# Kernel tuning notes

Hardware: AMD Instinct MI355X
Metric: run time of the kernel (lower is better)

## Reference

```python
import jax, jax.numpy as jnp
import numpy as np

B = 32768          # number of document embeddings
EMB = 768          # emb_size
M = 32             # subvector_num
K = 256            # subvector_cents = 2**subvector_bits
D = EMB // M       # last_dim per subvector = 24


def setup_inputs() -> dict:
    key = jax.random.key(0)
    k1, k2, k3 = jax.random.split(key, 3)
    x = jax.random.normal(k1, (B, EMB), dtype=jnp.float32)
    codebook = jax.random.normal(k2, (M, K, D), dtype=jnp.float32) * 0.05
    # OPQ rotation matrix (orthogonal-ish init; stored as a frozen Parameter in torch)
    rotate = jax.random.normal(k3, (EMB, EMB), dtype=jnp.float32) / np.sqrt(EMB)
    return {"x": x, "codebook": codebook, "rotate": rotate}


def reference(x, codebook, rotate):
    # OPQ: rotate embeddings first (torch: torch.matmul(cur_embeddings, self.rotate.T))
    xr = jnp.matmul(x, rotate.T)                      # [B, EMB]
    # Split into subvectors: [B, M, D]
    xs = xr.reshape(B, M, D)
    # dist_mode == 'ip': compute_scores = sum(a * b, -1) per subvector per centroid
    scores = jnp.einsum('bmd,mkd->bmk', xs, codebook)  # [B, M, K]
    return scores
```

## Files before the change

### kernel.cpp

```cpp
#include <hip/hip_runtime.h>
#include <hip/hip_bf16.h>

typedef __bf16 bf16;
typedef __bf16 bf16x4 __attribute__((ext_vector_type(4)));
typedef __bf16 bf16x8 __attribute__((ext_vector_type(8)));
typedef float f32x4 __attribute__((ext_vector_type(4)));

#define NB   32768
#define EMB  768
#define MSUB 32
#define KC   256
#define DSUB 24


__device__ __forceinline__ bf16x8 cvt8(float4 a, float4 b) {
    bf16x8 r;
    r[0] = (bf16)a.x; r[1] = (bf16)a.y; r[2] = (bf16)a.z; r[3] = (bf16)a.w;
    r[4] = (bf16)b.x; r[5] = (bf16)b.y; r[6] = (bf16)b.z; r[7] = (bf16)b.w;
    return r;
}

__device__ __forceinline__ void lds_barrier() {
    asm volatile("s_waitcnt lgkmcnt(0)" ::: "memory");
    __builtin_amdgcn_s_barrier();
    __builtin_amdgcn_sched_barrier(0);
}

__global__ __launch_bounds__(256, 4)
void pq_prep(const float* __restrict__ cb, const float* __restrict__ rot,
             bf16* __restrict__ cb_pad, bf16* __restrict__ rot_f) {
    const int b = blockIdx.x;
    const int t = threadIdx.x;
    if (b < 288) {
        const int o     = b * 2048 + t * 8;
        const int chunk = o >> 9;
        const int lane8 = o & 511;
        const int l15   = (lane8 >> 3) & 15;
        const int lg    = lane8 >> 7;
        const int jj    = (chunk / 24) * 16 + l15;
        const int ee    = (chunk % 24) * 32 + lg * 8;
        const float* rp = rot + (size_t)jj * EMB + ee;
        *(bf16x8*)(rot_f + o) = cvt8(*(const float4*)rp, *(const float4*)(rp + 4));
    } else {
        const int o  = (b - 288) * 2048 + t * 8;
        const int m  = o >> 13;
        const int k  = (o >> 5) & 255;
        const int d0 = o & 31;
        bf16x8 v;
        if (d0 < DSUB) {
            const float* cp = cb + (size_t)(m * KC + k) * DSUB + d0;
            v = cvt8(*(const float4*)cp, *(const float4*)(cp + 4));
        } else {
            const float4 fz = {0.f, 0.f, 0.f, 0.f};
            v = cvt8(fz, fz);
        }
        *(bf16x8*)(cb_pad + o) = v;
    }
}

__global__ __launch_bounds__(512, 4)
void pq_fused(const float* __restrict__ x, const bf16* __restrict__ rot_f,
              const bf16* __restrict__ cb_pad, float* __restrict__ out) {
    __shared__ __align__(16) char smem[81920];
    bf16*  xl  = (bf16*)smem;
    float* stg = (float*)(smem + 49152);

    const int tid  = threadIdx.x;
    const int w    = tid >> 6;
    const int lane = tid & 63;
    const int l15  = lane & 15;
    const int lg   = lane >> 4;

    const int bid = (int)blockIdx.x;
    const int swz = (bid & 7) * 128 + (bid >> 3);
    const int rowbase = swz * 32;

    #pragma unroll
    for (int i = 0; i < 6; ++i) {
        const int oct = i * 512 + tid;
        const int row = oct & 31;
        const int e8  = oct >> 5;
        const float* xp = x + (size_t)(rowbase + row) * EMB + e8 * 8;
        *(bf16x8*)&xl[(e8 * 32 + row) * 8] =
            cvt8(*(const float4*)xp, *(const float4*)(xp + 4));
    }
    __syncthreads();

    f32x4 acc[2][6];
    #pragma unroll
    for (int rt = 0; rt < 2; ++rt)
        #pragma unroll
        for (int jt = 0; jt < 6; ++jt)
            acc[rt][jt] = (f32x4){0.f, 0.f, 0.f, 0.f};

    const int jt0 = w * 6;
    #pragma unroll 2
    for (int et = 0; et < 24; ++et) {
        bf16x8 xfrag[2];
        #pragma unroll
        for (int rt = 0; rt < 2; ++rt)
            xfrag[rt] = *(const bf16x8*)&xl[(((et << 2) + lg) * 32 + rt * 16 + l15) * 8];
        #pragma unroll
        for (int jt = 0; jt < 6; ++jt) {
            const bf16* rp = rot_f + (((size_t)(jt0 + jt) * 24 + et) << 9) + lane * 8;
            bf16x8 rotfrag = *(const bf16x8*)rp;
            acc[0][jt] = __builtin_amdgcn_mfma_f32_16x16x32_bf16(rotfrag, xfrag[0], acc[0][jt], 0, 0, 0);
            acc[1][jt] = __builtin_amdgcn_mfma_f32_16x16x32_bf16(rotfrag, xfrag[1], acc[1][jt], 0, 0, 0);
        }
    }

    lds_barrier();

    const int jbase = w * 96;
    #pragma unroll
    for (int rt = 0; rt < 2; ++rt) {
        #pragma unroll
        for (int jt = 0; jt < 6; ++jt) {
            const int j0 = jbase + jt * 16 + lg * 4;
            const int m  = j0 / DSUB;
            const int d0 = j0 % DSUB;
            const int row = rt * 16 + l15;
            bf16x4 v;
            #pragma unroll
            for (int r = 0; r < 4; ++r) v[r] = (bf16)acc[rt][jt][r];
            *(bf16x4*)&xl[(m * 32 + row) * 24 + d0] = v;
        }
    }

    lds_barrier();

    const int rt = w >> 2;
    const int kb = (w & 3) * 4;
    const int hi = lg;
    const int srow = rt * 16 + l15;
    const int ssw  = (srow & 7) << 2;

    #pragma unroll 1
    for (int m = 0; m < MSUB; ++m) {
        int off = (m * 32 + srow) * 24 + hi * 8;
        off = off > 24568 ? 24568 : off;
        bf16x8 xfrag = *(const bf16x8*)&xl[off];

        const bf16* cbm = cb_pad + (size_t)m * (KC * 32);
        f32x4 a4[4];
        #pragma unroll
        for (int kk = 0; kk < 4; ++kk) {
            const int kt = kb + kk;
            bf16x8 cfrag = *(const bf16x8*)(cbm + (kt * 16 + l15) * 32 + hi * 8);
            a4[kk] = __builtin_amdgcn_mfma_f32_16x16x32_bf16(
                cfrag, xfrag, (f32x4){0.f, 0.f, 0.f, 0.f}, 0, 0, 0);
        }

        #pragma unroll
        for (int kk = 0; kk < 4; ++kk) {
            const int kidx = (((kb + kk) * 16 + hi * 4) ^ ssw);
            *(f32x4*)&stg[srow * 256 + kidx] = a4[kk];
        }

        lds_barrier();

        #pragma unroll
        for (int j = 0; j < 4; ++j) {
            const int drow = w * 4 + j;
            const int kidx = (4 * lane) ^ ((drow & 7) << 2);
            f32x4 v = *(const f32x4*)&stg[drow * 256 + kidx];
            *(f32x4*)(out + ((size_t)(rowbase + drow) * MSUB + m) * KC + 4 * lane) = v;
        }

        lds_barrier();
    }
}

extern "C" void kernel_launch(void* const* d_in, const int* in_sizes, int n_in,
                              void* d_out, int out_size, void* d_ws, size_t ws_size,
                              hipStream_t stream) {
    const float* x   = (const float*)d_in[0];
    const float* cbk = (const float*)d_in[1];
    const float* rot = (const float*)d_in[2];
    float* out = (float*)d_out;

    char* ws = (char*)d_ws;
    bf16* cb_pad = (bf16*)(ws);
    bf16* rot_f  = (bf16*)(ws + (1u << 20));

    hipLaunchKernelGGL(pq_prep,  dim3(416),  dim3(256), 0, stream, cbk, rot, cb_pad, rot_f);
    hipLaunchKernelGGL(pq_fused, dim3(1024), dim3(512), 0, stream, x, rot_f, cb_pad, out);
}
```

Before: 299.2 us.

## Process two row tiles per block and regroup score stage by subvector quads

Each block now handles 64 rows as two sequential 32-row tiles, which halves the grid. The score stage is reorganized so that each wave owns one of four subvectors and half of the centroids. Codebook fragments are loaded once per subvector group and reused across four 8-row groups, and each output row writes 4 KB of contiguous data instead of 1 KB. In exchange, half of each score MFMA's rows are duplicated and wasted, and the rotation GEMM is still recomputed for each tile.

```diff
diff --git a/kernel.cpp b/kernel.cpp
--- a/kernel.cpp
+++ b/kernel.cpp
@@ -59,8 +59,8 @@
 }
 
 __global__ __launch_bounds__(512, 4)
-void pq_fused(const float* __restrict__ x, const bf16* __restrict__ rot_f,
-              const bf16* __restrict__ cb_pad, float* __restrict__ out) {
+void pq_fused2(const float* __restrict__ x, const bf16* __restrict__ rot_f,
+               const bf16* __restrict__ cb_pad, float* __restrict__ out) {
     __shared__ __align__(16) char smem[81920];
     bf16*  xl  = (bf16*)smem;
     float* stg = (float*)(smem + 49152);
@@ -72,102 +72,116 @@
     const int lg   = lane >> 4;
 
     const int bid = (int)blockIdx.x;
-    const int swz = (bid & 7) * 128 + (bid >> 3);
-    const int rowbase = swz * 32;
-
-    #pragma unroll
-    for (int i = 0; i < 6; ++i) {
-        const int oct = i * 512 + tid;
-        const int row = oct & 31;
-        const int e8  = oct >> 5;
-        const float* xp = x + (size_t)(rowbase + row) * EMB + e8 * 8;
-        *(bf16x8*)&xl[(e8 * 32 + row) * 8] =
-            cvt8(*(const float4*)xp, *(const float4*)(xp + 4));
-    }
-    __syncthreads();
-
-    f32x4 acc[2][6];
-    #pragma unroll
-    for (int rt = 0; rt < 2; ++rt)
+    const int swz = (bid & 7) * 64 + (bid >> 3);
+
+    const int mi = w >> 1;
+    const int kh = w & 1;
+
+    #pragma unroll 1
+    for (int tt = 0; tt < 2; ++tt) {
+        const int rowbase = swz * 64 + tt * 32;
+
         #pragma unroll
-        for (int jt = 0; jt < 6; ++jt)
-            acc[rt][jt] = (f32x4){0.f, 0.f, 0.f, 0.f};
-
-    const int jt0 = w * 6;
-    #pragma unroll 2
-    for (int et = 0; et < 24; ++et) {
-        bf16x8 xfrag[2];
+        for (int i = 0; i < 6; ++i) {
+            const int oct = i * 512 + tid;
+            const int row = oct & 31;
+            const int e8  = oct >> 5;
+            const float* xp = x + (size_t)(rowbase + row) * EMB + e8 * 8;
+            *(bf16x8*)&xl[(e8 * 32 + row) * 8] =
+                cvt8(*(const float4*)xp, *(const float4*)(xp + 4));
+        }
+        lds_barrier();
+
+        f32x4 acc[2][6];
         #pragma unroll
         for (int rt = 0; rt < 2; ++rt)
-            xfrag[rt] = *(const bf16x8*)&xl[(((et << 2) + lg) * 32 + rt * 16 + l15) * 8];
+            #pragma unroll
+            for (int jt = 0; jt < 6; ++jt)
+                acc[rt][jt] = (f32x4){0.f, 0.f, 0.f, 0.f};
+
+        const int jt0 = w * 6;
+        #pragma unroll 2
+        for (int et = 0; et < 24; ++et) {
+            bf16x8 xfrag[2];
+            #pragma unroll
+            for (int rt = 0; rt < 2; ++rt)
+                xfrag[rt] = *(const bf16x8*)&xl[(((et << 2) + lg) * 32 + rt * 16 + l15) * 8];
+            #pragma unroll
+            for (int jt = 0; jt < 6; ++jt) {
+                const bf16* rp = rot_f + (((size_t)(jt0 + jt) * 24 + et) << 9) + lane * 8;
+                bf16x8 rotfrag = *(const bf16x8*)rp;
+                acc[0][jt] = __builtin_amdgcn_mfma_f32_16x16x32_bf16(rotfrag, xfrag[0], acc[0][jt], 0, 0, 0);
+                acc[1][jt] = __builtin_amdgcn_mfma_f32_16x16x32_bf16(rotfrag, xfrag[1], acc[1][jt], 0, 0, 0);
+            }
+        }
+
+        lds_barrier();
+
+        const int jbase = w * 96;
         #pragma unroll
-        for (int jt = 0; jt < 6; ++jt) {
-            const bf16* rp = rot_f + (((size_t)(jt0 + jt) * 24 + et) << 9) + lane * 8;
-            bf16x8 rotfrag = *(const bf16x8*)rp;
-            acc[0][jt] = __builtin_amdgcn_mfma_f32_16x16x32_bf16(rotfrag, xfrag[0], acc[0][jt], 0, 0, 0);
-            acc[1][jt] = __builtin_amdgcn_mfma_f32_16x16x32_bf16(rotfrag, xfrag[1], acc[1][jt], 0, 0, 0);
-        }
-    }
-
-    lds_barrier();
-
-    const int jbase = w * 96;
-    #pragma unroll
-    for (int rt = 0; rt < 2; ++rt) {
-        #pragma unroll
-        for (int jt = 0; jt < 6; ++jt) {
-            const int j0 = jbase + jt * 16 + lg * 4;
-            const int m  = j0 / DSUB;
-            const int d0 = j0 % DSUB;
-            const int row = rt * 16 + l15;
-            bf16x4 v;
-            #pragma unroll
-            for (int r = 0; r < 4; ++r) v[r] = (bf16)acc[rt][jt][r];
-            *(bf16x4*)&xl[(m * 32 + row) * 24 + d0] = v;
-        }
-    }
-
-    lds_barrier();
-
-    const int rt = w >> 2;
-    const int kb = (w & 3) * 4;
-    const int hi = lg;
-    const int srow = rt * 16 + l15;
-    const int ssw  = (srow & 7) << 2;
-
-    #pragma unroll 1
-    for (int m = 0; m < MSUB; ++m) {
-        int off = (m * 32 + srow) * 24 + hi * 8;
-        off = off > 24568 ? 24568 : off;
-        bf16x8 xfrag = *(const bf16x8*)&xl[off];
-
-        const bf16* cbm = cb_pad + (size_t)m * (KC * 32);
-        f32x4 a4[4];
-        #pragma unroll
-        for (int kk = 0; kk < 4; ++kk) {
-            const int kt = kb + kk;
-            bf16x8 cfrag = *(const bf16x8*)(cbm + (kt * 16 + l15) * 32 + hi * 8);
-            a4[kk] = __builtin_amdgcn_mfma_f32_16x16x32_bf16(
-                cfrag, xfrag, (f32x4){0.f, 0.f, 0.f, 0.f}, 0, 0, 0);
-        }
-
-        #pragma unroll
-        for (int kk = 0; kk < 4; ++kk) {
-            const int kidx = (((kb + kk) * 16 + hi * 4) ^ ssw);
-            *(f32x4*)&stg[srow * 256 + kidx] = a4[kk];
+        for (int rt = 0; rt < 2; ++rt) {
+            #pragma unroll
+            for (int jt = 0; jt < 6; ++jt) {
+                const int j0 = jbase + jt * 16 + lg * 4;
+                const int m  = j0 / DSUB;
+                const int d0 = j0 % DSUB;
+                const int row = rt * 16 + l15;
+                bf16x4 v;
+                #pragma unroll
+                for (int r = 0; r < 4; ++r) v[r] = (bf16)acc[rt][jt][r];
+                *(bf16x4*)&xl[(m * 32 + row) * 24 + d0] = v;
+            }
         }
 
         lds_barrier();
 
-        #pragma unroll
-        for (int j = 0; j < 4; ++j) {
-            const int drow = w * 4 + j;
-            const int kidx = (4 * lane) ^ ((drow & 7) << 2);
-            f32x4 v = *(const f32x4*)&stg[drow * 256 + kidx];
-            *(f32x4*)(out + ((size_t)(rowbase + drow) * MSUB + m) * KC + 4 * lane) = v;
-        }
-
-        lds_barrier();
+        #pragma unroll 1
+        for (int mg = 0; mg < 8; ++mg) {
+            const int m = mg * 4 + mi;
+
+            const bf16* cbm = cb_pad + (size_t)m * (KC * 32);
+            bf16x8 cfrag[8];
+            #pragma unroll
+            for (int kk = 0; kk < 8; ++kk)
+                cfrag[kk] = *(const bf16x8*)(cbm + ((kh * 8 + kk) * 16 + l15) * 32 + lg * 8);
+
+            #pragma unroll 1
+            for (int rg = 0; rg < 4; ++rg) {
+                int off = (m * 32 + rg * 8 + (l15 & 7)) * 24 + lg * 8;
+                off = off > 24568 ? 24568 : off;
+                bf16x8 xfrag = *(const bf16x8*)&xl[off];
+
+                f32x4 a8[8];
+                #pragma unroll
+                for (int kk = 0; kk < 8; ++kk)
+                    a8[kk] = __builtin_amdgcn_mfma_f32_16x16x32_bf16(
+                        cfrag[kk], xfrag, (f32x4){0.f, 0.f, 0.f, 0.f}, 0, 0, 0);
+
+                if (l15 < 8) {
+                    const int row = l15;
+                    #pragma unroll
+                    for (int kk = 0; kk < 8; ++kk) {
+                        const int col = mi * 256 + (kh * 8 + kk) * 16 + lg * 4;
+                        *(f32x4*)&stg[row * 1024 + (col ^ (row << 2))] = a8[kk];
+                    }
+                }
+
+                lds_barrier();
+
+                {
+                    const int row = w;
+                    float* op = out + ((size_t)(rowbase + rg * 8 + row) * MSUB + mg * 4) * KC;
+                    #pragma unroll
+                    for (int i = 0; i < 4; ++i) {
+                        const int c = i * 256 + 4 * lane;
+                        f32x4 v = *(const f32x4*)&stg[row * 1024 + (c ^ (row << 2))];
+                        *(f32x4*)(op + c) = v;
+                    }
+                }
+
+                lds_barrier();
+            }
+        }
     }
 }
 
@@ -183,6 +197,6 @@
     bf16* cb_pad = (bf16*)(ws);
     bf16* rot_f  = (bf16*)(ws + (1u << 20));
 
-    hipLaunchKernelGGL(pq_prep,  dim3(416),  dim3(256), 0, stream, cbk, rot, cb_pad, rot_f);
-    hipLaunchKernelGGL(pq_fused, dim3(1024), dim3(512), 0, stream, x, rot_f, cb_pad, out);
-}
+    hipLaunchKernelGGL(pq_prep,   dim3(416), dim3(256), 0, stream, cbk, rot, cb_pad, rot_f);
+    hipLaunchKernelGGL(pq_fused2, dim3(512), dim3(512), 0, stream, x, rot_f, cb_pad, out);
+}
```

New measurement: 360.6 us. 20.5% more time.

## Process two row tiles per block and prefetch the second tile's input during the first

Applied to the files above, without the earlier changes.

Each block now handles 64 rows as two 32-row tiles, launching half as many blocks. The second tile's x rows are loaded into registers before the first tile's codebook-score phase and written to LDS after it, so the global load latency overlaps compute and output stores. This costs 48 extra float registers per thread, which may reduce occupancy or cause spills, and halves the grid to 512 blocks, which could underfill the GPU.

```diff
diff --git a/kernel.cpp b/kernel.cpp
--- a/kernel.cpp
+++ b/kernel.cpp
@@ -59,8 +59,8 @@
 }
 
 __global__ __launch_bounds__(512, 4)
-void pq_fused(const float* __restrict__ x, const bf16* __restrict__ rot_f,
-              const bf16* __restrict__ cb_pad, float* __restrict__ out) {
+void pq_fused5(const float* __restrict__ x, const bf16* __restrict__ rot_f,
+               const bf16* __restrict__ cb_pad, float* __restrict__ out) {
     __shared__ __align__(16) char smem[81920];
     bf16*  xl  = (bf16*)smem;
     float* stg = (float*)(smem + 49152);
@@ -72,103 +72,134 @@
     const int lg   = lane >> 4;
 
     const int bid = (int)blockIdx.x;
-    const int swz = (bid & 7) * 128 + (bid >> 3);
-    const int rowbase = swz * 32;
+    const int swz = (bid & 7) * 64 + (bid >> 3);
+    const int rowbase0 = swz * 64;
+    const int rowbase1 = swz * 64 + 32;
+
+    auto stageA_gemm = [&]() {
+        f32x4 acc[2][6];
+        #pragma unroll
+        for (int rt = 0; rt < 2; ++rt)
+            #pragma unroll
+            for (int jt = 0; jt < 6; ++jt)
+                acc[rt][jt] = (f32x4){0.f, 0.f, 0.f, 0.f};
+
+        const int jt0 = w * 6;
+        #pragma unroll 2
+        for (int et = 0; et < 24; ++et) {
+            bf16x8 xfrag[2];
+            #pragma unroll
+            for (int rt = 0; rt < 2; ++rt)
+                xfrag[rt] = *(const bf16x8*)&xl[(((et << 2) + lg) * 32 + rt * 16 + l15) * 8];
+            #pragma unroll
+            for (int jt = 0; jt < 6; ++jt) {
+                const bf16* rp = rot_f + (((size_t)(jt0 + jt) * 24 + et) << 9) + lane * 8;
+                bf16x8 rotfrag = *(const bf16x8*)rp;
+                acc[0][jt] = __builtin_amdgcn_mfma_f32_16x16x32_bf16(rotfrag, xfrag[0], acc[0][jt], 0, 0, 0);
+                acc[1][jt] = __builtin_amdgcn_mfma_f32_16x16x32_bf16(rotfrag, xfrag[1], acc[1][jt], 0, 0, 0);
+            }
+        }
+
+        lds_barrier();
+
+        const int jbase = w * 96;
+        #pragma unroll
+        for (int rt = 0; rt < 2; ++rt) {
+            #pragma unroll
+            for (int jt = 0; jt < 6; ++jt) {
+                const int j0 = jbase + jt * 16 + lg * 4;
+                const int m  = j0 / DSUB;
+                const int d0 = j0 % DSUB;
+                const int row = rt * 16 + l15;
+                bf16x4 v;
+                #pragma unroll
+                for (int r = 0; r < 4; ++r) v[r] = (bf16)acc[rt][jt][r];
+                *(bf16x4*)&xl[(m * 32 + row) * 24 + d0] = v;
+            }
+        }
+
+        lds_barrier();
+    };
+
+    auto phaseB = [&](int rowbase) {
+        const int rt = w >> 2;
+        const int kb = (w & 3) * 4;
+        const int hi = lg;
+        const int srow = rt * 16 + l15;
+        const int ssw  = (srow & 7) << 2;
+
+        #pragma unroll 1
+        for (int m = 0; m < MSUB; ++m) {
+            int off = (m * 32 + srow) * 24 + hi * 8;
+            off = off > 24568 ? 24568 : off;
+            bf16x8 xfrag = *(const bf16x8*)&xl[off];
+
+            const bf16* cbm = cb_pad + (size_t)m * (KC * 32);
+            f32x4 a4[4];
+            #pragma unroll
+            for (int kk = 0; kk < 4; ++kk) {
+                const int kt = kb + kk;
+                bf16x8 cfrag = *(const bf16x8*)(cbm + (kt * 16 + l15) * 32 + hi * 8);
+                a4[kk] = __builtin_amdgcn_mfma_f32_16x16x32_bf16(
+                    cfrag, xfrag, (f32x4){0.f, 0.f, 0.f, 0.f}, 0, 0, 0);
+            }
+
+            #pragma unroll
+            for (int kk = 0; kk < 4; ++kk) {
+                const int kidx = (((kb + kk) * 16 + hi * 4) ^ ssw);
+                *(f32x4*)&stg[srow * 256 + kidx] = a4[kk];
+            }
+
+            lds_barrier();
+
+            #pragma unroll
+            for (int j = 0; j < 4; ++j) {
+                const int drow = w * 4 + j;
+                const int kidx = (4 * lane) ^ ((drow & 7) << 2);
+                f32x4 v = *(const f32x4*)&stg[drow * 256 + kidx];
+                *(f32x4*)(out + ((size_t)(rowbase + drow) * MSUB + m) * KC + 4 * lane) = v;
+            }
+
+            lds_barrier();
+        }
+    };
 
     #pragma unroll
     for (int i = 0; i < 6; ++i) {
         const int oct = i * 512 + tid;
         const int row = oct & 31;
         const int e8  = oct >> 5;
-        const float* xp = x + (size_t)(rowbase + row) * EMB + e8 * 8;
+        const float* xp = x + (size_t)(rowbase0 + row) * EMB + e8 * 8;
         *(bf16x8*)&xl[(e8 * 32 + row) * 8] =
             cvt8(*(const float4*)xp, *(const float4*)(xp + 4));
     }
     __syncthreads();
-
-    f32x4 acc[2][6];
+    stageA_gemm();
+
+    float4 pf[12];
     #pragma unroll
-    for (int rt = 0; rt < 2; ++rt)
-        #pragma unroll
-        for (int jt = 0; jt < 6; ++jt)
-            acc[rt][jt] = (f32x4){0.f, 0.f, 0.f, 0.f};
-
-    const int jt0 = w * 6;
-    #pragma unroll 2
-    for (int et = 0; et < 24; ++et) {
-        bf16x8 xfrag[2];
-        #pragma unroll
-        for (int rt = 0; rt < 2; ++rt)
-            xfrag[rt] = *(const bf16x8*)&xl[(((et << 2) + lg) * 32 + rt * 16 + l15) * 8];
-        #pragma unroll
-        for (int jt = 0; jt < 6; ++jt) {
-            const bf16* rp = rot_f + (((size_t)(jt0 + jt) * 24 + et) << 9) + lane * 8;
-            bf16x8 rotfrag = *(const bf16x8*)rp;
-            acc[0][jt] = __builtin_amdgcn_mfma_f32_16x16x32_bf16(rotfrag, xfrag[0], acc[0][jt], 0, 0, 0);
-            acc[1][jt] = __builtin_amdgcn_mfma_f32_16x16x32_bf16(rotfrag, xfrag[1], acc[1][jt], 0, 0, 0);
-        }
-    }
-
+    for (int i = 0; i < 6; ++i) {
+        const int oct = i * 512 + tid;
+        const int row = oct & 31;
+        const int e8  = oct >> 5;
+        const float* xp = x + (size_t)(rowbase1 + row) * EMB + e8 * 8;
+        pf[2 * i]     = *(const float4*)(xp);
+        pf[2 * i + 1] = *(const float4*)(xp + 4);
+    }
+
+    phaseB(rowbase0);
+
+    #pragma unroll
+    for (int i = 0; i < 6; ++i) {
+        const int oct = i * 512 + tid;
+        const int row = oct & 31;
+        const int e8  = oct >> 5;
+        *(bf16x8*)&xl[(e8 * 32 + row) * 8] = cvt8(pf[2 * i], pf[2 * i + 1]);
+    }
     lds_barrier();
-
-    const int jbase = w * 96;
-    #pragma unroll
-    for (int rt = 0; rt < 2; ++rt) {
-        #pragma unroll
-        for (int jt = 0; jt < 6; ++jt) {
-            const int j0 = jbase + jt * 16 + lg * 4;
-            const int m  = j0 / DSUB;
-            const int d0 = j0 % DSUB;
-            const int row = rt * 16 + l15;
-            bf16x4 v;
-            #pragma unroll
-            for (int r = 0; r < 4; ++r) v[r] = (bf16)acc[rt][jt][r];
-            *(bf16x4*)&xl[(m * 32 + row) * 24 + d0] = v;
-        }
-    }
-
-    lds_barrier();
-
-    const int rt = w >> 2;
-    const int kb = (w & 3) * 4;
-    const int hi = lg;
-    const int srow = rt * 16 + l15;
-    const int ssw  = (srow & 7) << 2;
-
-    #pragma unroll 1
-    for (int m = 0; m < MSUB; ++m) {
-        int off = (m * 32 + srow) * 24 + hi * 8;
-        off = off > 24568 ? 24568 : off;
-        bf16x8 xfrag = *(const bf16x8*)&xl[off];
-
-        const bf16* cbm = cb_pad + (size_t)m * (KC * 32);
-        f32x4 a4[4];
-        #pragma unroll
-        for (int kk = 0; kk < 4; ++kk) {
-            const int kt = kb + kk;
-            bf16x8 cfrag = *(const bf16x8*)(cbm + (kt * 16 + l15) * 32 + hi * 8);
-            a4[kk] = __builtin_amdgcn_mfma_f32_16x16x32_bf16(
-                cfrag, xfrag, (f32x4){0.f, 0.f, 0.f, 0.f}, 0, 0, 0);
-        }
-
-        #pragma unroll
-        for (int kk = 0; kk < 4; ++kk) {
-            const int kidx = (((kb + kk) * 16 + hi * 4) ^ ssw);
-            *(f32x4*)&stg[srow * 256 + kidx] = a4[kk];
-        }
-
-        lds_barrier();
-
-        #pragma unroll
-        for (int j = 0; j < 4; ++j) {
-            const int drow = w * 4 + j;
-            const int kidx = (4 * lane) ^ ((drow & 7) << 2);
-            f32x4 v = *(const f32x4*)&stg[drow * 256 + kidx];
-            *(f32x4*)(out + ((size_t)(rowbase + drow) * MSUB + m) * KC + 4 * lane) = v;
-        }
-
-        lds_barrier();
-    }
+    stageA_gemm();
+
+    phaseB(rowbase1);
 }
 
 extern "C" void kernel_launch(void* const* d_in, const int* in_sizes, int n_in,
@@ -183,6 +214,6 @@
     bf16* cb_pad = (bf16*)(ws);
     bf16* rot_f  = (bf16*)(ws + (1u << 20));
 
-    hipLaunchKernelGGL(pq_prep,  dim3(416),  dim3(256), 0, stream, cbk, rot, cb_pad, rot_f);
-    hipLaunchKernelGGL(pq_fused, dim3(1024), dim3(512), 0, stream, x, rot_f, cb_pad, out);
-}
+    hipLaunchKernelGGL(pq_prep,   dim3(416), dim3(256), 0, stream, cbk, rot, cb_pad, rot_f);
+    hipLaunchKernelGGL(pq_fused5, dim3(512), dim3(512), 0, stream, x, rot_f, cb_pad, out);
+}
```

New measurement: 330.1 us. 10.3% more time.
